# Optimization experiments

Measured on AMD Instinct MI355X. Metric: run time of the kernel, lower is better.

The kernel has to match this reference:

```python
import jax, jax.numpy as jnp
import numpy as np

NUM_TILES = 64
N_EVENTS = 16777216  # routing events per update()


def setup_inputs() -> dict:
    key = jax.random.key(0)
    k1, k2 = jax.random.split(key)
    prev_tiles = jax.random.randint(k1, (N_EVENTS,), 0, NUM_TILES, dtype=jnp.int64 if jax.config.jax_enable_x64 else jnp.int32)
    curr_tiles = jax.random.randint(k2, (N_EVENTS,), 0, NUM_TILES, dtype=jnp.int64 if jax.config.jax_enable_x64 else jnp.int32)
    transitions = jnp.zeros((NUM_TILES, NUM_TILES), dtype=jnp.float32)
    total_transitions = jnp.zeros((), dtype=jnp.float32)
    return {
        "prev_tiles": prev_tiles,
        "curr_tiles": curr_tiles,
        "transitions": transitions,
        "total_transitions": total_transitions,
    }


def reference(prev_tiles, curr_tiles, transitions, total_transitions):
    """Vectorized TopologyTracker.update(): histogram of (prev, curr) pairs.

    Equivalent to: for p, c in zip(prev, curr): transitions[p, c] += 1
    """
    T = transitions.shape[0]
    # Flatten pair index into a single histogram bin id: p * T + c
    flat_idx = prev_tiles.reshape(-1) * T + curr_tiles.reshape(-1)
    counts = jax.ops.segment_sum(
        jnp.ones_like(flat_idx, dtype=transitions.dtype), flat_idx, num_segments=T * T
    ).reshape(T, T)
    new_transitions = transitions + counts
    new_total = total_transitions + jnp.asarray(prev_tiles.size, dtype=total_transitions.dtype)
    return new_transitions, new_total
```

## Files before the change

### kernel.cpp

```cpp
#include <hip/hip_runtime.h>

#define BINS 4096
#define HIST_BLOCKS 1024
#define HIST_THREADS 512

__global__ void topo_init_kernel(const float* __restrict__ transitions,
                                 const float* __restrict__ total,
                                 float* __restrict__ out,
                                 float n_events_f, int bins) {
    int i = blockIdx.x * blockDim.x + threadIdx.x;
    if (i < bins) out[i] = transitions[i];
    if (i == 0) out[bins] = total[0] + n_events_f;
}

__global__ void __launch_bounds__(HIST_THREADS)
topo_hist_kernel(const int* __restrict__ prev,
                 const int* __restrict__ curr,
                 float* __restrict__ out, int n) {
    __shared__ unsigned int h[BINS];
    for (int i = threadIdx.x; i < BINS; i += HIST_THREADS) h[i] = 0u;
    __syncthreads();

    const int n4 = n >> 2;
    const int4* __restrict__ p4 = (const int4*)prev;
    const int4* __restrict__ c4 = (const int4*)curr;

    const int base   = blockIdx.x * (HIST_THREADS * 2) + threadIdx.x;
    const int stride = gridDim.x * (HIST_THREADS * 2);

    for (int i = base; i < n4; i += stride) {
        const int j = i + HIST_THREADS;
        int4 p0 = p4[i];
        int4 c0 = c4[i];
        int4 p1, c1;
        const bool ok = (j < n4);
        if (ok) { p1 = p4[j]; c1 = c4[j]; }

        atomicAdd(&h[(p0.x << 6) | c0.x], 1u);
        atomicAdd(&h[(p0.y << 6) | c0.y], 1u);
        atomicAdd(&h[(p0.z << 6) | c0.z], 1u);
        atomicAdd(&h[(p0.w << 6) | c0.w], 1u);
        if (ok) {
            atomicAdd(&h[(p1.x << 6) | c1.x], 1u);
            atomicAdd(&h[(p1.y << 6) | c1.y], 1u);
            atomicAdd(&h[(p1.z << 6) | c1.z], 1u);
            atomicAdd(&h[(p1.w << 6) | c1.w], 1u);
        }
    }
    for (int i = (n4 << 2) + blockIdx.x * HIST_THREADS + threadIdx.x; i < n;
         i += gridDim.x * HIST_THREADS) {
        atomicAdd(&h[(prev[i] << 6) | curr[i]], 1u);
    }

    __syncthreads();
    for (int i = threadIdx.x; i < BINS; i += HIST_THREADS) {
        unsigned int c = h[i];
        if (c) atomicAdd(&out[i], (float)c);
    }
}

extern "C" void kernel_launch(void* const* d_in, const int* in_sizes, int n_in,
                              void* d_out, int out_size, void* d_ws, size_t ws_size,
                              hipStream_t stream) {
    const int*   prev        = (const int*)d_in[0];
    const int*   curr        = (const int*)d_in[1];
    const float* transitions = (const float*)d_in[2];
    const float* total       = (const float*)d_in[3];
    float* out = (float*)d_out;

    const int n    = in_sizes[0];
    const int bins = in_sizes[2];

    int init_blocks = (bins + 1 + 255) / 256;
    topo_init_kernel<<<init_blocks, 256, 0, stream>>>(transitions, total, out,
                                                      (float)n, bins);

    topo_hist_kernel<<<HIST_BLOCKS, HIST_THREADS, 0, stream>>>(prev, curr, out, n);
}
```

Measured before the change: 154.6 us.

## Replace global float atomics with per-block partial histograms plus reduction kernel

Each histogram block now writes its full shared-memory histogram to a workspace buffer with vectorized stores, instead of issuing float atomicAdds to the output. A separate reduce kernel sums the partials per bin across block groups and does a small number of atomics. The block/thread shape also changes to 512 blocks of 1024 threads. This removes heavy global atomic contention on 4096 bins but adds an 8 MB workspace write/read and an extra kernel launch.

```diff
diff --git a/kernel.cpp b/kernel.cpp
--- a/kernel.cpp
+++ b/kernel.cpp
@@ -1,8 +1,12 @@
 #include <hip/hip_runtime.h>
 
 #define BINS 4096
-#define HIST_BLOCKS 1024
-#define HIST_THREADS 512
+#define HIST_BLOCKS 512
+#define HIST_THREADS 1024
+
+#define RED_TPB 256
+#define RED_BG  (BINS / RED_TPB)
+#define RED_PG  16
 
 __global__ void topo_init_kernel(const float* __restrict__ transitions,
                                  const float* __restrict__ total,
@@ -16,7 +20,9 @@
 __global__ void __launch_bounds__(HIST_THREADS)
 topo_hist_kernel(const int* __restrict__ prev,
                  const int* __restrict__ curr,
-                 float* __restrict__ out, int n) {
+                 float* __restrict__ out,
+                 unsigned int* __restrict__ ws,
+                 int n, int use_ws) {
     __shared__ unsigned int h[BINS];
     for (int i = threadIdx.x; i < BINS; i += HIST_THREADS) h[i] = 0u;
     __syncthreads();
@@ -53,10 +59,34 @@
     }
 
     __syncthreads();
-    for (int i = threadIdx.x; i < BINS; i += HIST_THREADS) {
-        unsigned int c = h[i];
-        if (c) atomicAdd(&out[i], (float)c);
+
+    if (use_ws) {
+        uint4* __restrict__ dst = (uint4*)(ws + (size_t)blockIdx.x * BINS);
+        for (int t = threadIdx.x; t < (BINS >> 2); t += HIST_THREADS) {
+            dst[t] = *reinterpret_cast<const uint4*>(&h[t << 2]);
+        }
+    } else {
+        for (int i = threadIdx.x; i < BINS; i += HIST_THREADS) {
+            unsigned int c = h[i];
+            if (c) atomicAdd(&out[i], (float)c);
+        }
     }
+}
+
+__global__ void __launch_bounds__(RED_TPB)
+topo_reduce_kernel(const unsigned int* __restrict__ ws,
+                   float* __restrict__ out, int nparts) {
+    const int bg  = blockIdx.x % RED_BG;
+    const int pg  = blockIdx.x / RED_BG;
+    const int bin = bg * RED_TPB + threadIdx.x;
+
+    const int pp = (nparts + RED_PG - 1) / RED_PG;
+    const int p0 = pg * pp;
+    const int p1 = (p0 + pp < nparts) ? (p0 + pp) : nparts;
+
+    unsigned int s = 0;
+    for (int p = p0; p < p1; ++p) s += ws[(size_t)p * BINS + bin];
+    if (s) atomicAdd(&out[bin], (float)s);
 }
 
 extern "C" void kernel_launch(void* const* d_in, const int* in_sizes, int n_in,
@@ -71,9 +101,18 @@
     const int n    = in_sizes[0];
     const int bins = in_sizes[2];
 
+    const size_t ws_needed = (size_t)HIST_BLOCKS * BINS * sizeof(unsigned int);
+    const int use_ws = (d_ws != nullptr && ws_size >= ws_needed) ? 1 : 0;
+
     int init_blocks = (bins + 1 + 255) / 256;
     topo_init_kernel<<<init_blocks, 256, 0, stream>>>(transitions, total, out,
                                                       (float)n, bins);
 
-    topo_hist_kernel<<<HIST_BLOCKS, HIST_THREADS, 0, stream>>>(prev, curr, out, n);
+    topo_hist_kernel<<<HIST_BLOCKS, HIST_THREADS, 0, stream>>>(
+        prev, curr, out, (unsigned int*)d_ws, n, use_ws);
+
+    if (use_ws) {
+        topo_reduce_kernel<<<RED_BG * RED_PG, RED_TPB, 0, stream>>>(
+            (const unsigned int*)d_ws, out, HIST_BLOCKS);
+    }
 }
```

After: 159.4 us. 1.03x slower.
